# Performance work log

Measured on AMD Instinct MI355X. Metric: run time of the kernel, lower is better.

The kernel has to match this reference:

```python
import jax, jax.numpy as jnp
import numpy as np

B, T, U, V, C, K = 64, 800, 64, 60, 512, 10

def setup_inputs() -> dict:
    key = jax.random.key(0)
    ks = jax.random.split(key, 8)
    x = jax.random.normal(ks[0], (B, T, 3), dtype=jnp.float32)
    char_ids = jax.random.randint(ks[1], (B, U), 0, V)
    onehots = jax.nn.one_hot(char_ids, V, dtype=jnp.float32)  # [B,U,V]
    text_lens = jax.random.randint(ks[2], (B, 1), 32, U + 1).astype(jnp.float32)
    w_old = jnp.zeros((B, V), jnp.float32)
    kappa_old = jnp.zeros((B, K), jnp.float32)
    prev_h = jnp.zeros((B, C), jnp.float32)
    prev_c = jnp.zeros((B, C), jnp.float32)
    s = 0.08
    W_ih = jax.random.normal(ks[3], (4 * C, 3 + V), jnp.float32) * s
    W_hh = jax.random.normal(ks[4], (4 * C, C), jnp.float32) * s
    b_ih = jnp.zeros((4 * C,), jnp.float32)
    b_hh = jnp.zeros((4 * C,), jnp.float32)
    win_W = jax.random.normal(ks[5], (3 * K, C), jnp.float32) * s
    win_b = jnp.zeros((3 * K,), jnp.float32)
    return dict(x=x, onehots=onehots, text_lens=text_lens, w_old=w_old,
                kappa_old=kappa_old, prev_h=prev_h, prev_c=prev_c,
                W_ih=W_ih, W_hh=W_hh, b_ih=b_ih, b_hh=b_hh,
                win_W=win_W, win_b=win_b)

def reference(x, onehots, text_lens, w_old, kappa_old, prev_h, prev_c,
              W_ih, W_hh, b_ih, b_hh, win_W, win_b):
    Upad = onehots.shape[1]
    idx = jnp.arange(Upad + 1, dtype=x.dtype)          # text-position indices
    scale = Upad / text_lens                           # [B,1] length normalization

    def step(carry, xt):
        h, c, w, kap = carry
        inp = jnp.concatenate([xt, w], axis=-1)        # [B, 3+V]
        gates = inp @ W_ih.T + b_ih + h @ W_hh.T + b_hh
        i, f, g, o = jnp.split(gates, 4, axis=-1)
        i = jax.nn.sigmoid(i); f = jax.nn.sigmoid(f)
        g = jnp.tanh(g);      o = jax.nn.sigmoid(o)
        c = f * c + i * g
        h = o * jnp.tanh(c)
        # Gaussian-mixture attention window
        p = jnp.exp(h @ win_W.T + win_b)               # [B, 3K]
        alpha, beta, dkap = jnp.split(p, 3, axis=-1)   # each [B, K]
        kap = kap + dkap
        gravity = -beta[:, :, None] * (kap[:, :, None] - idx) ** 2   # [B,K,U+1]
        phi = jnp.sum(alpha[:, :, None] * jnp.exp(gravity), axis=1) * scale  # [B,U+1]
        w = jnp.einsum('bu,buv->bv', phi[:, :Upad], onehots)
        return (h, c, w, kap), (h, w, phi)

    xs = jnp.swapaxes(x, 0, 1)                         # [T,B,3]
    (h, c, w, kap), (hs, ws, phis) = jax.lax.scan(
        step, (prev_h, prev_c, w_old, kappa_old), xs)
    ws = jnp.swapaxes(ws, 0, 1)                        # [B,T,V]
    hs = jnp.swapaxes(hs, 0, 1)                        # [B,T,C]
    return ws, hs, h, c, w, kap, phis[-1]
```

## Files before the change

### kernel.cpp

```cpp
#include <hip/hip_runtime.h>
#include <math.h>

#define B_  64
#define T_  800
#define U_  64
#define V_  60
#define C_  512
#define K_  10
#define KX  576
#define NWG 256
#define NTH 512
#define KQ  8
#define KSL 72
#define NB  4
#define GRPWG 16

__device__ __forceinline__ float sigm(float v)  { return 1.f/(1.f+__expf(-v)); }
__device__ __forceinline__ float tanhx(float v) { return 1.f - 2.f/(__expf(2.f*v)+1.f); }

__launch_bounds__(NTH, 2)
__global__ void lstm_attn_persistent(
    const float* __restrict__ x,
    const float* __restrict__ onehots,
    const float* __restrict__ text_lens,
    const float* __restrict__ w_old,
    const float* __restrict__ kappa_old,
    const float* __restrict__ prev_h,
    const float* __restrict__ prev_c,
    const float* __restrict__ W_ih,
    const float* __restrict__ W_hh,
    const float* __restrict__ b_ih,
    const float* __restrict__ b_hh,
    const float* __restrict__ win_W,
    const float* __restrict__ win_b,
    unsigned long long* __restrict__ hpair,
    float* __restrict__ out)
{
  const long OUT_WS  = 0;
  const long OUT_HS  = (long)B_*T_*V_;
  const long OUT_H   = OUT_HS + (long)B_*T_*C_;
  const long OUT_C   = OUT_H  + (long)B_*C_;
  const long OUT_W   = OUT_C  + (long)B_*C_;
  const long OUT_KAP = OUT_W  + (long)B_*V_;
  const long OUT_PHI = OUT_KAP+ (long)B_*K_;

  const int tid  = threadIdx.x;
  const int kq   = tid >> 6;
  const int lane = tid & 63;
  const int bid  = blockIdx.x;
  const int grp  = bid & 15;
  const int gblk = bid >> 4;
  const int b0   = grp * NB;

  __shared__ __align__(16) float hx[NB][KX];
  __shared__ __align__(16) float part[KQ][NB][2][68];
  __shared__ float p_lds[NB][32];
  __shared__ float kap_lds[NB][12];
  __shared__ float scale_lds[NB];
  __shared__ int   ids_lds[NB][64];

  float Wreg[2][KSL];
  float bias2[2];
  #pragma unroll
  for (int s = 0; s < 2; ++s) {
    int gp   = gblk*128 + lane + 64*s;
    int gate = gp & 3;
    int ch   = gp >> 2;
    int row  = gate*C_ + ch;
    #pragma unroll
    for (int i = 0; i < KSL; ++i) {
      int k = kq*KSL + i;
      float v;
      if      (k < 3)  v = W_ih[row*63 + k];
      else if (k == 3) v = 0.f;
      else if (k < 64) v = W_ih[row*63 + (k-1)];
      else             v = W_hh[row*C_ + (k-64)];
      Wreg[s][i] = v;
    }
    bias2[s] = b_ih[row] + b_hh[row];
  }

  const int wj   = lane % 30;
  const int wh   = (lane < 60) ? (lane / 30) : 0;
  float winreg[32];
  #pragma unroll
  for (int i = 0; i < 32; ++i)
    winreg[i] = win_W[wj*C_ + kq*64 + wh*32 + i];

  const int ub    = tid >> 5;
  const int chloc = tid & 31;
  const int mych  = gblk*32 + chloc;
  float c_reg = 0.f;
  if (tid < 128) c_reg = prev_c[(long)(b0 + ub)*C_ + mych];

  float winb_r = (tid < 120) ? win_b[tid % 30] : 0.f;

  for (int i = tid; i < NB*KX; i += NTH) {
    int bb = i / KX, k = i % KX;
    int b = b0 + bb;
    float v;
    if      (k < 3)  v = x[((long)b*T_ + 0)*3 + k];
    else if (k < 4)  v = 0.f;
    else if (k < 64) v = w_old[b*V_ + (k-4)];
    else             v = prev_h[(long)b*C_ + (k-64)];
    hx[bb][k] = v;
  }
  for (int i = tid; i < NB*K_; i += NTH)
    kap_lds[i/K_][i%K_] = kappa_old[(b0 + i/K_)*K_ + i%K_];
  if (tid < NB) scale_lds[tid] = (float)U_ / text_lens[b0 + tid];
  for (int i = tid; i < NB*U_; i += NTH) {
    int bb = i / U_, u = i % U_;
    const float* oh = onehots + ((long)(b0+bb)*U_ + u)*V_;
    int best = 0; float bv = oh[0];
    for (int vv = 1; vv < V_; ++vv) { float q = oh[vv]; if (q > bv) { bv = q; best = vv; } }
    ids_lds[bb][u] = best;
  }
  __syncthreads();

  for (int t = 0; t < T_; ++t) {
    float acc[NB][2];
    #pragma unroll
    for (int bb = 0; bb < NB; ++bb) {
      acc[bb][0] = (kq == 0) ? bias2[0] : 0.f;
      acc[bb][1] = (kq == 0) ? bias2[1] : 0.f;
    }
    #pragma unroll
    for (int bb = 0; bb < NB; ++bb) {
      const float* hxb = &hx[bb][kq*KSL];
      float a0 = acc[bb][0], a1 = acc[bb][1];
      #pragma unroll
      for (int i4 = 0; i4 < KSL/4; ++i4) {
        float4 h4 = *(const float4*)(hxb + i4*4);
        a0 = fmaf(Wreg[0][i4*4+0], h4.x, a0);
        a0 = fmaf(Wreg[0][i4*4+1], h4.y, a0);
        a0 = fmaf(Wreg[0][i4*4+2], h4.z, a0);
        a0 = fmaf(Wreg[0][i4*4+3], h4.w, a0);
        a1 = fmaf(Wreg[1][i4*4+0], h4.x, a1);
        a1 = fmaf(Wreg[1][i4*4+1], h4.y, a1);
        a1 = fmaf(Wreg[1][i4*4+2], h4.z, a1);
        a1 = fmaf(Wreg[1][i4*4+3], h4.w, a1);
      }
      acc[bb][0] = a0; acc[bb][1] = a1;
    }
    #pragma unroll
    for (int bb = 0; bb < NB; ++bb) {
      part[kq][bb][0][lane] = acc[bb][0];
      part[kq][bb][1][lane] = acc[bb][1];
    }
    __syncthreads();

    if (tid < 128) {
      const int sr = chloc >> 4, c4 = (chloc & 15) * 4;
      float4 s = make_float4(0.f, 0.f, 0.f, 0.f);
      #pragma unroll
      for (int q = 0; q < KQ; ++q) {
        float4 v = *(const float4*)&part[q][ub][sr][c4];
        s.x += v.x; s.y += v.y; s.z += v.z; s.w += v.w;
      }
      float ig = sigm(s.x), fg = sigm(s.y), gg = tanhx(s.z), og = sigm(s.w);
      float c = fg*c_reg + ig*gg;
      c_reg = c;
      float h = og * tanhx(c);
      int b = b0 + ub;
      unsigned long long pk =
          ((unsigned long long)(unsigned)(t+1) << 32) | (unsigned long long)__float_as_uint(h);
      __hip_atomic_store(&hpair[(long)(t&1)*B_*C_ + (long)b*C_ + mych], pk,
                         __ATOMIC_RELAXED, __HIP_MEMORY_SCOPE_AGENT);
      out[OUT_HS + ((long)b*T_ + t)*C_ + mych] = h;
      if (t == T_-1) {
        out[OUT_H + (long)b*C_ + mych] = h;
        out[OUT_C + (long)b*C_ + mych] = c;
      }
    } else if (tid < 368) {
      int s0 = tid - 128;
      hx[s0/60][4 + s0%60] = 0.f;
    } else if (tid < 384) {
      int i = tid - 368, bb = i >> 2, k = i & 3;
      int tn = t + 1;
      hx[bb][k] = (k < 3 && tn < T_) ? x[((long)(b0+bb)*T_ + tn)*3 + k] : 0.f;
    }

    {
      const unsigned long long* src = hpair + (long)(t&1)*B_*C_;
      const long base = (long)b0*C_ + tid*4;
      const int want = t + 1;
      unsigned long long v0, v1, v2, v3;
      while (true) {
        v0 = __hip_atomic_load(&src[base+0], __ATOMIC_RELAXED, __HIP_MEMORY_SCOPE_AGENT);
        v1 = __hip_atomic_load(&src[base+1], __ATOMIC_RELAXED, __HIP_MEMORY_SCOPE_AGENT);
        v2 = __hip_atomic_load(&src[base+2], __ATOMIC_RELAXED, __HIP_MEMORY_SCOPE_AGENT);
        v3 = __hip_atomic_load(&src[base+3], __ATOMIC_RELAXED, __HIP_MEMORY_SCOPE_AGENT);
        if ((int)(v0 >> 32) >= want && (int)(v1 >> 32) >= want &&
            (int)(v2 >> 32) >= want && (int)(v3 >> 32) >= want) break;
      }
      int off = tid * 4;
      int bb = off >> 9, k = off & 511;
      *(float4*)&hx[bb][64 + k] = make_float4(
          __uint_as_float((unsigned)v0), __uint_as_float((unsigned)v1),
          __uint_as_float((unsigned)v2), __uint_as_float((unsigned)v3));
    }
    __syncthreads();

    #pragma unroll
    for (int bb = 0; bb < NB; ++bb) {
      const float* hb = &hx[bb][64 + kq*64 + wh*32];
      float a = 0.f;
      #pragma unroll
      for (int i4 = 0; i4 < 8; ++i4) {
        float4 h4 = *(const float4*)(hb + i4*4);
        a = fmaf(winreg[i4*4+0], h4.x, a);
        a = fmaf(winreg[i4*4+1], h4.y, a);
        a = fmaf(winreg[i4*4+2], h4.z, a);
        a = fmaf(winreg[i4*4+3], h4.w, a);
      }
      if (lane < 60) part[kq][bb][0][lane] = a;
    }
    __syncthreads();

    if (tid < 120) {
      int bb = tid / 30, j = tid % 30;
      float s = 0.f;
      #pragma unroll
      for (int q = 0; q < KQ; ++q) s += part[q][bb][0][j] + part[q][bb][0][30+j];
      float p = __expf(s + winb_r);
      p_lds[bb][j] = p;
      if (j >= 20) {
        float nk = kap_lds[bb][j-20] + p;
        kap_lds[bb][j-20] = nk;
        if (t == T_-1 && gblk == 0) out[OUT_KAP + (b0+bb)*K_ + (j-20)] = nk;
      }
    }
    __syncthreads();

    if (kq < NB) {
      int bb = kq, u = lane;
      float s = 0.f;
      float uf = (float)u;
      #pragma unroll
      for (int k = 0; k < K_; ++k) {
        float d = kap_lds[bb][k] - uf;
        s += p_lds[bb][k] * __expf(-p_lds[bb][10+k]*d*d);
      }
      float phiv = s * scale_lds[bb];
      atomicAdd(&hx[bb][4 + ids_lds[bb][u]], phiv);
      if (t == T_-1 && gblk == 0) out[OUT_PHI + (b0+bb)*65 + u] = phiv;
    }
    if (t == T_-1 && gblk == 0 && tid < NB) {
      int b2 = tid;
      float s2 = 0.f;
      #pragma unroll
      for (int k = 0; k < K_; ++k) {
        float d = kap_lds[b2][k] - 64.f;
        s2 += p_lds[b2][k] * __expf(-p_lds[b2][10+k]*d*d);
      }
      out[OUT_PHI + (b0+b2)*65 + 64] = s2 * scale_lds[b2];
    }
    __syncthreads();

    if (gblk == (t & 15) && tid < 240) {
      int bb = tid / 60, v = tid % 60;
      float wv = hx[bb][4+v];
      out[OUT_WS + ((long)(b0+bb)*T_ + t)*V_ + v] = wv;
      if (t == T_-1) out[OUT_W + (b0+bb)*V_ + v] = wv;
    }
  }
}

extern "C" void kernel_launch(void* const* d_in, const int* in_sizes, int n_in,
                              void* d_out, int out_size, void* d_ws, size_t ws_size,
                              hipStream_t stream) {
  const float* x         = (const float*)d_in[0];
  const float* onehots   = (const float*)d_in[1];
  const float* text_lens = (const float*)d_in[2];
  const float* w_old     = (const float*)d_in[3];
  const float* kappa_old = (const float*)d_in[4];
  const float* prev_h    = (const float*)d_in[5];
  const float* prev_c    = (const float*)d_in[6];
  const float* W_ih      = (const float*)d_in[7];
  const float* W_hh      = (const float*)d_in[8];
  const float* b_ih      = (const float*)d_in[9];
  const float* b_hh      = (const float*)d_in[10];
  const float* win_W     = (const float*)d_in[11];
  const float* win_b     = (const float*)d_in[12];
  unsigned long long* hpair = (unsigned long long*)d_ws;
  float* out = (float*)d_out;

  hipMemsetAsync(d_ws, 0, 2ull*B_*C_*sizeof(unsigned long long), stream);

  lstm_attn_persistent<<<NWG, NTH, 0, stream>>>(
      x, onehots, text_lens, w_old, kappa_old, prev_h, prev_c,
      W_ih, W_hh, b_ih, b_hh, win_W, win_b, hpair, out);
}
```

Before: 4.392 ms.

## Compute window projection from local h slices and exchange partial sums

Each workgroup now computes its partial attention-window projection from its own 32 freshly computed h channels. It publishes the 120 partial sums through a second flag-tagged global buffer, so the window matmul no longer has to wait for the full h exchange and the per-block reduction drops out. LSTM and window weights are stored in registers as packed half2 to cut register pressure, which adds fp16 rounding error to the gate and window results. The h gather is split so half the threads poll h and others poll window partials concurrently, with 8 values per thread.

```diff
diff --git a/kernel.cpp b/kernel.cpp
--- a/kernel.cpp
+++ b/kernel.cpp
@@ -1,4 +1,5 @@
 #include <hip/hip_runtime.h>
+#include <hip/hip_fp16.h>
 #include <math.h>
 
 #define B_  64
@@ -14,6 +15,11 @@
 #define KSL 72
 #define NB  4
 #define GRPWG 16
+
+typedef unsigned long long ull;
+
+#define WP_OFF 65536
+#define WP_STRIDE 128
 
 __device__ __forceinline__ float sigm(float v)  { return 1.f/(1.f+__expf(-v)); }
 __device__ __forceinline__ float tanhx(float v) { return 1.f - 2.f/(__expf(2.f*v)+1.f); }
@@ -33,7 +39,7 @@
     const float* __restrict__ b_hh,
     const float* __restrict__ win_W,
     const float* __restrict__ win_b,
-    unsigned long long* __restrict__ hpair,
+    ull* __restrict__ wsb,
     float* __restrict__ out)
 {
   const long OUT_WS  = 0;
@@ -54,46 +60,60 @@
 
   __shared__ __align__(16) float hx[NB][KX];
   __shared__ __align__(16) float part[KQ][NB][2][68];
+  __shared__ __align__(16) float hown[NB][32];
+  __shared__ float wp_lds[GRPWG][120];
   __shared__ float p_lds[NB][32];
   __shared__ float kap_lds[NB][12];
   __shared__ float scale_lds[NB];
   __shared__ int   ids_lds[NB][64];
 
-  float Wreg[2][KSL];
+  __half2 Wh2[KSL];
   float bias2[2];
-  #pragma unroll
-  for (int s = 0; s < 2; ++s) {
-    int gp   = gblk*128 + lane + 64*s;
-    int gate = gp & 3;
-    int ch   = gp >> 2;
-    int row  = gate*C_ + ch;
+  {
     #pragma unroll
     for (int i = 0; i < KSL; ++i) {
-      int k = kq*KSL + i;
-      float v;
-      if      (k < 3)  v = W_ih[row*63 + k];
-      else if (k == 3) v = 0.f;
-      else if (k < 64) v = W_ih[row*63 + (k-1)];
-      else             v = W_hh[row*C_ + (k-64)];
-      Wreg[s][i] = v;
-    }
-    bias2[s] = b_ih[row] + b_hh[row];
-  }
-
-  const int wj   = lane % 30;
-  const int wh   = (lane < 60) ? (lane / 30) : 0;
-  float winreg[32];
-  #pragma unroll
-  for (int i = 0; i < 32; ++i)
-    winreg[i] = win_W[wj*C_ + kq*64 + wh*32 + i];
+      float wv[2];
+      #pragma unroll
+      for (int s = 0; s < 2; ++s) {
+        int gp   = gblk*128 + lane + 64*s;
+        int gate = gp & 3;
+        int ch   = gp >> 2;
+        int row  = gate*C_ + ch;
+        int k = kq*KSL + i;
+        float v;
+        if      (k < 3)  v = W_ih[row*63 + k];
+        else if (k == 3) v = 0.f;
+        else if (k < 64) v = W_ih[row*63 + (k-1)];
+        else             v = W_hh[row*C_ + (k-64)];
+        wv[s] = v;
+      }
+      Wh2[i] = __floats2half2_rn(wv[0], wv[1]);
+    }
+    #pragma unroll
+    for (int s = 0; s < 2; ++s) {
+      int gp   = gblk*128 + lane + 64*s;
+      int gate = gp & 3;
+      int ch   = gp >> 2;
+      int row  = gate*C_ + ch;
+      bias2[s] = b_ih[row] + b_hh[row];
+    }
+  }
+
+  __half2 winw2[16];
+  if (tid < 120) {
+    int j = tid % 30;
+    #pragma unroll
+    for (int c2 = 0; c2 < 16; ++c2)
+      winw2[c2] = __floats2half2_rn(win_W[j*C_ + gblk*32 + 2*c2],
+                                    win_W[j*C_ + gblk*32 + 2*c2 + 1]);
+  }
+  float winb_r = (tid < 120) ? win_b[tid % 30] : 0.f;
 
   const int ub    = tid >> 5;
   const int chloc = tid & 31;
   const int mych  = gblk*32 + chloc;
   float c_reg = 0.f;
   if (tid < 128) c_reg = prev_c[(long)(b0 + ub)*C_ + mych];
-
-  float winb_r = (tid < 120) ? win_b[tid % 30] : 0.f;
 
   for (int i = tid; i < NB*KX; i += NTH) {
     int bb = i / KX, k = i % KX;
@@ -117,6 +137,9 @@
   }
   __syncthreads();
 
+  ull* hpair = wsb;
+  ull* wpair = wsb + WP_OFF;
+
   for (int t = 0; t < T_; ++t) {
     float acc[NB][2];
     #pragma unroll
@@ -131,14 +154,14 @@
       #pragma unroll
       for (int i4 = 0; i4 < KSL/4; ++i4) {
         float4 h4 = *(const float4*)(hxb + i4*4);
-        a0 = fmaf(Wreg[0][i4*4+0], h4.x, a0);
-        a0 = fmaf(Wreg[0][i4*4+1], h4.y, a0);
-        a0 = fmaf(Wreg[0][i4*4+2], h4.z, a0);
-        a0 = fmaf(Wreg[0][i4*4+3], h4.w, a0);
-        a1 = fmaf(Wreg[1][i4*4+0], h4.x, a1);
-        a1 = fmaf(Wreg[1][i4*4+1], h4.y, a1);
-        a1 = fmaf(Wreg[1][i4*4+2], h4.z, a1);
-        a1 = fmaf(Wreg[1][i4*4+3], h4.w, a1);
+        float2 w0 = __half22float2(Wh2[i4*4+0]);
+        float2 w1 = __half22float2(Wh2[i4*4+1]);
+        float2 w2 = __half22float2(Wh2[i4*4+2]);
+        float2 w3 = __half22float2(Wh2[i4*4+3]);
+        a0 = fmaf(w0.x, h4.x, a0);  a1 = fmaf(w0.y, h4.x, a1);
+        a0 = fmaf(w1.x, h4.y, a0);  a1 = fmaf(w1.y, h4.y, a1);
+        a0 = fmaf(w2.x, h4.z, a0);  a1 = fmaf(w2.y, h4.z, a1);
+        a0 = fmaf(w3.x, h4.w, a0);  a1 = fmaf(w3.y, h4.w, a1);
       }
       acc[bb][0] = a0; acc[bb][1] = a1;
     }
@@ -162,8 +185,8 @@
       c_reg = c;
       float h = og * tanhx(c);
       int b = b0 + ub;
-      unsigned long long pk =
-          ((unsigned long long)(unsigned)(t+1) << 32) | (unsigned long long)__float_as_uint(h);
+      hown[ub][chloc] = h;
+      ull pk = ((ull)(unsigned)(t+1) << 32) | (ull)__float_as_uint(h);
       __hip_atomic_store(&hpair[(long)(t&1)*B_*C_ + (long)b*C_ + mych], pk,
                          __ATOMIC_RELAXED, __HIP_MEMORY_SCOPE_AGENT);
       out[OUT_HS + ((long)b*T_ + t)*C_ + mych] = h;
@@ -179,41 +202,71 @@
       int tn = t + 1;
       hx[bb][k] = (k < 3 && tn < T_) ? x[((long)(b0+bb)*T_ + tn)*3 + k] : 0.f;
     }
-
-    {
-      const unsigned long long* src = hpair + (long)(t&1)*B_*C_;
-      const long base = (long)b0*C_ + tid*4;
+    __syncthreads();
+
+    if (tid < 120) {
+      int bb = tid / 30;
+      float s = 0.f;
+      const float4* h4p = (const float4*)&hown[bb][0];
+      #pragma unroll
+      for (int q = 0; q < 8; ++q) {
+        float4 hv = h4p[q];
+        float2 wa = __half22float2(winw2[2*q]);
+        float2 wb = __half22float2(winw2[2*q+1]);
+        s = fmaf(wa.x, hv.x, s); s = fmaf(wa.y, hv.y, s);
+        s = fmaf(wb.x, hv.z, s); s = fmaf(wb.y, hv.w, s);
+      }
+      ull pk = ((ull)(unsigned)(t+1) << 32) | (ull)__float_as_uint(s);
+      __hip_atomic_store(&wpair[(((long)(t&1)*16 + grp)*GRPWG + gblk)*WP_STRIDE + tid],
+                         pk, __ATOMIC_RELAXED, __HIP_MEMORY_SCOPE_AGENT);
+    }
+
+    if (tid < 240) {
+      const ull* src = wpair + ((long)(t&1)*16 + grp)*GRPWG*WP_STRIDE;
       const int want = t + 1;
-      unsigned long long v0, v1, v2, v3;
+      int wg_[8], i_[8];
+      long a_[8];
+      #pragma unroll
+      for (int q = 0; q < 8; ++q) {
+        int c = tid*8 + q;
+        wg_[q] = c / 120; i_[q] = c % 120;
+        a_[q] = (long)wg_[q]*WP_STRIDE + i_[q];
+      }
+      ull v[8];
       while (true) {
-        v0 = __hip_atomic_load(&src[base+0], __ATOMIC_RELAXED, __HIP_MEMORY_SCOPE_AGENT);
-        v1 = __hip_atomic_load(&src[base+1], __ATOMIC_RELAXED, __HIP_MEMORY_SCOPE_AGENT);
-        v2 = __hip_atomic_load(&src[base+2], __ATOMIC_RELAXED, __HIP_MEMORY_SCOPE_AGENT);
-        v3 = __hip_atomic_load(&src[base+3], __ATOMIC_RELAXED, __HIP_MEMORY_SCOPE_AGENT);
-        if ((int)(v0 >> 32) >= want && (int)(v1 >> 32) >= want &&
-            (int)(v2 >> 32) >= want && (int)(v3 >> 32) >= want) break;
-      }
-      int off = tid * 4;
+        bool ok = true;
+        #pragma unroll
+        for (int q = 0; q < 8; ++q) {
+          v[q] = __hip_atomic_load(&src[a_[q]], __ATOMIC_RELAXED, __HIP_MEMORY_SCOPE_AGENT);
+          ok &= ((int)(v[q] >> 32) >= want);
+        }
+        if (ok) break;
+      }
+      #pragma unroll
+      for (int q = 0; q < 8; ++q)
+        wp_lds[wg_[q]][i_[q]] = __uint_as_float((unsigned)v[q]);
+    } else if (tid >= 256) {
+      const int tid2 = tid - 256;
+      const ull* hsrc = hpair + (long)(t&1)*B_*C_ + (long)b0*C_ + (long)tid2*8;
+      const int want = t + 1;
+      ull v[8];
+      while (true) {
+        bool ok = true;
+        #pragma unroll
+        for (int q = 0; q < 8; ++q) {
+          v[q] = __hip_atomic_load(&hsrc[q], __ATOMIC_RELAXED, __HIP_MEMORY_SCOPE_AGENT);
+          ok &= ((int)(v[q] >> 32) >= want);
+        }
+        if (ok) break;
+      }
+      int off = tid2 * 8;
       int bb = off >> 9, k = off & 511;
       *(float4*)&hx[bb][64 + k] = make_float4(
-          __uint_as_float((unsigned)v0), __uint_as_float((unsigned)v1),
-          __uint_as_float((unsigned)v2), __uint_as_float((unsigned)v3));
-    }
-    __syncthreads();
-
-    #pragma unroll
-    for (int bb = 0; bb < NB; ++bb) {
-      const float* hb = &hx[bb][64 + kq*64 + wh*32];
-      float a = 0.f;
-      #pragma unroll
-      for (int i4 = 0; i4 < 8; ++i4) {
-        float4 h4 = *(const float4*)(hb + i4*4);
-        a = fmaf(winreg[i4*4+0], h4.x, a);
-        a = fmaf(winreg[i4*4+1], h4.y, a);
-        a = fmaf(winreg[i4*4+2], h4.z, a);
-        a = fmaf(winreg[i4*4+3], h4.w, a);
-      }
-      if (lane < 60) part[kq][bb][0][lane] = a;
+          __uint_as_float((unsigned)v[0]), __uint_as_float((unsigned)v[1]),
+          __uint_as_float((unsigned)v[2]), __uint_as_float((unsigned)v[3]));
+      *(float4*)&hx[bb][64 + k + 4] = make_float4(
+          __uint_as_float((unsigned)v[4]), __uint_as_float((unsigned)v[5]),
+          __uint_as_float((unsigned)v[6]), __uint_as_float((unsigned)v[7]));
     }
     __syncthreads();
 
@@ -221,7 +274,7 @@
       int bb = tid / 30, j = tid % 30;
       float s = 0.f;
       #pragma unroll
-      for (int q = 0; q < KQ; ++q) s += part[q][bb][0][j] + part[q][bb][0][30+j];
+      for (int wg = 0; wg < GRPWG; ++wg) s += wp_lds[wg][tid];
       float p = __expf(s + winb_r);
       p_lds[bb][j] = p;
       if (j >= 20) {
@@ -282,12 +335,12 @@
   const float* b_hh      = (const float*)d_in[10];
   const float* win_W     = (const float*)d_in[11];
   const float* win_b     = (const float*)d_in[12];
-  unsigned long long* hpair = (unsigned long long*)d_ws;
+  ull*   wsb = (ull*)d_ws;
   float* out = (float*)d_out;
 
-  hipMemsetAsync(d_ws, 0, 2ull*B_*C_*sizeof(unsigned long long), stream);
+  hipMemsetAsync(d_ws, 0, 1048576, stream);
 
   lstm_attn_persistent<<<NWG, NTH, 0, stream>>>(
       x, onehots, text_lens, w_old, kappa_old, prev_h, prev_c,
-      W_ih, W_hh, b_ih, b_hh, win_W, win_b, hpair, out);
+      W_ih, W_hh, b_ih, b_hh, win_W, win_b, wsb, out);
 }
```

After: 6.351 ms. 44.6% more time.
